# Kernel tuning notes

Measured on AMD Instinct MI355X. Metric: run time of the kernel, lower is better.

Reference implementation:

```python
import jax, jax.numpy as jnp
import numpy as np

N, T, D, H = 128, 128, 1024, 1024


def setup_inputs() -> dict:
    key = jax.random.key(0)
    ks = jax.random.split(key, 5)
    x = jax.random.normal(ks[0], (N, T, D), dtype=jnp.float32)
    A = jax.random.normal(ks[1], (N, H, 4, 4), dtype=jnp.float32)
    Wx = jax.random.normal(ks[2], (D, 4 * H), dtype=jnp.float32) / np.sqrt(D)
    Wh = jax.random.normal(ks[3], (H, 4 * H), dtype=jnp.float32) / np.sqrt(H)
    Wattn = jax.random.normal(ks[4], (H, 4 * H), dtype=jnp.float32) / np.sqrt(H)
    b = jnp.zeros((4 * H,), dtype=jnp.float32)
    return {"x": x, "A": A, "Wx": Wx, "Wh": Wh, "Wattn": Wattn, "b": b}


def reference(x, A, Wx, Wh, Wattn, b):
    n, t, d = x.shape
    h_dim = A.shape[1]
    scale = 1.0 / (h_dim ** 0.5)
    A_flat = A.reshape(n, h_dim, 16)            # (N, H, 16) flattened 4x4 grid
    h0 = A_flat.mean(axis=2)                    # mean-pooled feature init
    c0 = h0

    def step(carry, xt):
        h, c = carry
        # scaled dot-product attention over the 16 spatial positions
        scores = jnp.einsum('nh,nhp->np', h, A_flat) * scale   # (N, 16)
        w = jax.nn.softmax(scores, axis=-1)
        attn = jnp.einsum('nhp,np->nh', A_flat, w)             # (N, H)
        # fused gate pre-activations
        a = h @ Wh + xt @ Wx + attn @ Wattn + b                # (N, 4H)
        ai, af, ao, ag = jnp.split(a, 4, axis=1)
        i = jax.nn.sigmoid(ai)
        f = jax.nn.sigmoid(af)
        o = jax.nn.sigmoid(ao)
        g = jnp.tanh(ag)
        nc = f * c + i * g
        nh = o * jnp.tanh(nc)
        return (nh, nc), nh

    _, hs = jax.lax.scan(step, (h0, c0), jnp.transpose(x, (1, 0, 2)))
    return jnp.transpose(hs, (1, 0, 2))         # (N, T, H)
```

## Files before the change

kernel.cpp:

```cpp
#include <hip/hip_runtime.h>
#include <hip/hip_bf16.h>


typedef __bf16 bf16x8 __attribute__((ext_vector_type(8)));
typedef float f32x4 __attribute__((ext_vector_type(4)));

__device__ __forceinline__ unsigned short f2bf(float f) {
    unsigned int u = __float_as_uint(f);
    u += 0x7FFFu + ((u >> 16) & 1u);
    return (unsigned short)(u >> 16);
}
__device__ __forceinline__ float bf2f(unsigned short u) {
    return __uint_as_float(((unsigned int)u) << 16);
}
__device__ __forceinline__ float sigf(float x) { return 1.0f / (1.0f + __expf(-x)); }
__device__ __forceinline__ float tanhf_fast(float x) {
    const float t = __expf(-2.0f * fabsf(x));
    const float r = (1.0f - t) / (1.0f + t);
    return copysignf(r, x);
}

__global__ __launch_bounds__(256) void k_build_wtf2(
    const float* __restrict__ Wh, const float* __restrict__ Wx,
    unsigned short* __restrict__ WTf) {
    __shared__ float tile[64][65];
    const int cs2 = blockIdx.x;
    const int kq  = blockIdx.y;
    const int tid = threadIdx.x;
#pragma unroll
    for (int it = 0; it < 16; ++it) {
        int idx = it * 256 + tid;
        int kl = idx >> 6, cl = idx & 63;
        int col = cs2 * 64 + cl;
        int j = (col & 3) * 1024 + (col >> 2);
        int k = kq * 64 + kl;
        tile[kl][cl] = (k < 1024) ? Wh[(size_t)k * 4096 + j]
                                  : Wx[(size_t)(k - 1024) * 4096 + j];
    }
    __syncthreads();
#pragma unroll
    for (int it = 0; it < 2; ++it) {
        int slotid = it * 256 + tid;
        int l   = slotid & 63;
        int cf  = (slotid >> 6) & 1;
        int ksl = (slotid >> 7) & 1;
        int sl  = slotid >> 8;
        int s = cs2 * 2 + sl, ks = kq * 2 + ksl;
        int clocal = sl * 32 + cf * 16 + (l & 15);
        int klocal = ksl * 32 + ((l >> 4) << 3);
        unsigned short v[8];
#pragma unroll
        for (int i = 0; i < 8; ++i) v[i] = f2bf(tile[klocal + i][clocal]);
        *(int4*)&WTf[(size_t)(((s * 64 + ks) * 2 + cf) * 64 + l) * 8] = *(const int4*)v;
    }
}

__global__ __launch_bounds__(256) void k_build_waf(
    const float* __restrict__ Wattn, unsigned short* __restrict__ WAf) {
    __shared__ float tile[64][65];
    const int cs2 = blockIdx.x;
    const int kq  = blockIdx.y;
    const int tid = threadIdx.x;
#pragma unroll
    for (int it = 0; it < 16; ++it) {
        int idx = it * 256 + tid;
        int kl = idx >> 6, cl = idx & 63;
        int col = cs2 * 64 + cl;
        int j = (col & 3) * 1024 + (col >> 2);
        int k = kq * 64 + kl;
        tile[kl][cl] = Wattn[(size_t)k * 4096 + j];
    }
    __syncthreads();
#pragma unroll
    for (int it = 0; it < 2; ++it) {
        int slotid = it * 256 + tid;
        int l   = slotid & 63;
        int cf  = (slotid >> 6) & 1;
        int ksl = (slotid >> 7) & 1;
        int sl  = slotid >> 8;
        int s = cs2 * 2 + sl, ks = kq * 2 + ksl;
        int clocal = sl * 32 + cf * 16 + (l & 15);
        int klocal = ksl * 32 + ((l >> 4) << 3);
        unsigned short v[8];
#pragma unroll
        for (int i = 0; i < 8; ++i) v[i] = f2bf(tile[klocal + i][clocal]);
        *(int4*)&WAf[(size_t)(((s * 32 + ks) * 2 + cf) * 64 + l) * 8] = *(const int4*)v;
    }
}

__global__ __launch_bounds__(256) void k_pack_at(
    const float* __restrict__ Ag, unsigned short* __restrict__ ATf) {
    __shared__ unsigned short lds[1024][17];
    const int n = blockIdx.x;
    const int tid = threadIdx.x;
#pragma unroll
    for (int it = 0; it < 16; ++it) {
        int idx = it * 256 + tid;
        const float4 v = ((const float4*)(Ag + (size_t)n * 16384))[idx];
        int flat = idx * 4;
        int u = flat >> 4, p = flat & 15;
        lds[u][p + 0] = f2bf(v.x); lds[u][p + 1] = f2bf(v.y);
        lds[u][p + 2] = f2bf(v.z); lds[u][p + 3] = f2bf(v.w);
    }
    __syncthreads();
#pragma unroll
    for (int it = 0; it < 8; ++it) {
        int slot = it * 256 + tid;
        int kc = slot >> 6, l = slot & 63;
        int ubase = kc * 32 + ((l >> 4) << 3);
        int p = l & 15;
        unsigned short v[8];
#pragma unroll
        for (int i = 0; i < 8; ++i) v[i] = lds[ubase + i][p];
        *(int4*)&ATf[((size_t)n * 2048 + slot) * 8] = *(const int4*)v;
    }
}

__global__ __launch_bounds__(512) void k_aw_gemm(
    const unsigned short* __restrict__ ATf, const unsigned short* __restrict__ WAf,
    unsigned short* __restrict__ AW) {
    const int ng = blockIdx.x;
    const int ct = blockIdx.y;
    const int tid = threadIdx.x;
    const int lane = tid & 63, wave = tid >> 6;
    const int s = ct * 4 + (wave >> 1), cf = wave & 1;
    const int n0 = ng * 8;
    f32x4 acc[8] = {};
    const unsigned short* bp = WAf + ((size_t)((s * 32) * 2 + cf) * 64 + lane) * 8;
    const unsigned short* ap = ATf + ((size_t)n0 * 2048 + lane) * 8;
#pragma unroll 4
    for (int kc = 0; kc < 32; ++kc) {
        bf16x8 bf = *(const bf16x8*)(bp + (size_t)kc * 1024);
#pragma unroll
        for (int nn = 0; nn < 8; ++nn) {
            bf16x8 af = *(const bf16x8*)(ap + (size_t)nn * 16384 + (size_t)kc * 512);
            acc[nn] = __builtin_amdgcn_mfma_f32_16x16x32_bf16(af, bf, acc[nn], 0, 0, 0);
        }
    }
    const int col = ct * 128 + wave * 16 + (lane & 15);
    const int prow = (lane >> 4) << 2;
#pragma unroll
    for (int nn = 0; nn < 8; ++nn) {
        ushort4 st = make_ushort4(f2bf(acc[nn][0]), f2bf(acc[nn][1]),
                                  f2bf(acc[nn][2]), f2bf(acc[nn][3]));
        *(ushort4*)&AW[((size_t)(n0 + nn) * 4096 + col) * 16 + prow] = st;
    }
}

__global__ __launch_bounds__(512) void k_build_aw(
    const float* __restrict__ Wattn, const float* __restrict__ Ag,
    unsigned short* __restrict__ AW) {
    extern __shared__ float Alds[];
    const int jt = blockIdx.x;
    const int ng = blockIdx.y;
    const int tid = threadIdx.x;
    const int jl = tid & 127, pg = tid >> 7;
    const int jj = jt * 128 + jl;
    for (int nn = 0; nn < 16; ++nn) {
        const int n = ng * 16 + nn;
        __syncthreads();
#pragma unroll
        for (int q = 0; q < 8; ++q) {
            int idx = q * 512 + tid;
            ((float4*)Alds)[idx] = ((const float4*)(Ag + (size_t)n * 16384))[idx];
        }
        __syncthreads();
        f32x4 acc = {0.f, 0.f, 0.f, 0.f};
#pragma unroll 8
        for (int u = 0; u < 1024; ++u) {
            float wv = Wattn[(size_t)u * 4096 + jj];
            const float4 av = *(const float4*)&Alds[u * 16 + pg * 4];
            acc[0] += wv * av.x; acc[1] += wv * av.y;
            acc[2] += wv * av.z; acc[3] += wv * av.w;
        }
        const int g = jj >> 10, unit = jj & 1023;
        const int cre = unit * 4 + g;
        ushort4 st = make_ushort4(f2bf(acc[0]), f2bf(acc[1]), f2bf(acc[2]), f2bf(acc[3]));
        *(ushort4*)&AW[((size_t)n * 4096 + cre) * 16 + pg * 4] = st;
    }
}

__global__ __launch_bounds__(512) void k_init(
    const float* __restrict__ Ag, float* __restrict__ cst,
    unsigned short* __restrict__ hF0, float* __restrict__ sp) {
    const int n = blockIdx.x;
    const int t = threadIdx.x;
    float contrib[16];
#pragma unroll
    for (int p = 0; p < 16; ++p) contrib[p] = 0.f;
#pragma unroll
    for (int e = 0; e < 2; ++e) {
        const int u = t * 2 + e;
        const float4* ap = (const float4*)&Ag[((size_t)n * 1024 + u) * 16];
        float4 a0 = ap[0], a1 = ap[1], a2 = ap[2], a3 = ap[3];
        float s = a0.x + a0.y + a0.z + a0.w + a1.x + a1.y + a1.z + a1.w +
                  a2.x + a2.y + a2.z + a2.w + a3.x + a3.y + a3.z + a3.w;
        float h0 = s * (1.0f / 16.0f);
        cst[n * 1024 + u] = h0;
        const int rfg = n >> 4, kc = u >> 5, l = (n & 15) | (((u >> 3) & 3) << 4);
        hF0[(size_t)((rfg * 32 + kc) * 64 + l) * 8 + (u & 7)] = f2bf(h0);
        contrib[0]  += h0 * a0.x;  contrib[1]  += h0 * a0.y;
        contrib[2]  += h0 * a0.z;  contrib[3]  += h0 * a0.w;
        contrib[4]  += h0 * a1.x;  contrib[5]  += h0 * a1.y;
        contrib[6]  += h0 * a1.z;  contrib[7]  += h0 * a1.w;
        contrib[8]  += h0 * a2.x;  contrib[9]  += h0 * a2.y;
        contrib[10] += h0 * a2.z;  contrib[11] += h0 * a2.w;
        contrib[12] += h0 * a3.x;  contrib[13] += h0 * a3.y;
        contrib[14] += h0 * a3.z;  contrib[15] += h0 * a3.w;
    }
#pragma unroll
    for (int p = 0; p < 16; ++p) {
        contrib[p] += __shfl_xor(contrib[p], 1);
        contrib[p] += __shfl_xor(contrib[p], 2);
    }
    if ((t & 3) == 0) {
        const int slice = t >> 2;
        float4* dst = (float4*)&sp[(size_t)n * 4096 + slice * 16];
        dst[0] = make_float4(contrib[0], contrib[1], contrib[2], contrib[3]);
        dst[1] = make_float4(contrib[4], contrib[5], contrib[6], contrib[7]);
        dst[2] = make_float4(contrib[8], contrib[9], contrib[10], contrib[11]);
        dst[3] = make_float4(contrib[12], contrib[13], contrib[14], contrib[15]);
    }
    *(float4*)&sp[(size_t)n * 4096 + 2048 + t * 4] = make_float4(0.f, 0.f, 0.f, 0.f);
}

__global__ __launch_bounds__(64) void k_soft(
    const float* __restrict__ spin, float* __restrict__ w_ws,
    const float* __restrict__ x, unsigned short* __restrict__ xf, int ts) {
    __shared__ float sq[16];
    const int n = blockIdx.x;
    const int lane = threadIdx.x;
    f32x4 acc = {0.f, 0.f, 0.f, 0.f};
    const float4* base = (const float4*)(spin + (size_t)n * 4096);
#pragma unroll
    for (int it = 0; it < 16; ++it) {
        const float4 v = base[it * 64 + lane];
        acc[0] += v.x; acc[1] += v.y; acc[2] += v.z; acc[3] += v.w;
    }
#pragma unroll
    for (int m = 4; m <= 32; m <<= 1) {
        acc[0] += __shfl_xor(acc[0], m);
        acc[1] += __shfl_xor(acc[1], m);
        acc[2] += __shfl_xor(acc[2], m);
        acc[3] += __shfl_xor(acc[3], m);
    }
    if (lane < 4) *(float4*)&sq[lane * 4] = make_float4(acc[0], acc[1], acc[2], acc[3]);
    __syncthreads();
    if (lane < 16) {
        const float s = sq[lane] * 0.03125f;
        float mx = s;
#pragma unroll
        for (int m = 1; m < 16; m <<= 1) mx = fmaxf(mx, __shfl_xor(mx, m));
        const float e = __expf(s - mx);
        float se = e;
#pragma unroll
        for (int m = 1; m < 16; m <<= 1) se += __shfl_xor(se, m);
        w_ws[n * 16 + lane] = e / se;
    }
    const float4* xp = (const float4*)&x[((size_t)n * 128 + ts) * 1024];
#pragma unroll
    for (int i = 0; i < 2; ++i) {
        const int js = lane * 2 + i;
        const float4 x0 = xp[js * 2], x1 = xp[js * 2 + 1];
        unsigned short v[8] = {f2bf(x0.x), f2bf(x0.y), f2bf(x0.z), f2bf(x0.w),
                               f2bf(x1.x), f2bf(x1.y), f2bf(x1.z), f2bf(x1.w)};
        const int j0 = js * 8;
        const int l = (n & 15) | (((j0 >> 3) & 3) << 4);
        *(int4*)&xf[(size_t)(((n >> 4) * 32 + (j0 >> 5)) * 64 + l) * 8] = *(const int4*)v;
    }
}

__global__ __launch_bounds__(512, 4) void k_step(
    const unsigned short* __restrict__ WTf, const unsigned short* __restrict__ AW,
    const unsigned short* __restrict__ hFin, unsigned short* __restrict__ hFout,
    const unsigned short* __restrict__ xf,
    const float* __restrict__ w_ws, float* __restrict__ spout,
    float* __restrict__ cst, const float* __restrict__ Ag,
    const float* __restrict__ bias4, float* __restrict__ out, int ts) {
    __shared__ float wlds[64][17];
    __shared__ float accred[2048];
    const int bid0 = blockIdx.x;
    const int lid = (bid0 & 7) * 64 + (bid0 >> 3);
    const int cs16 = lid >> 1, rh = lid & 1;
    const int tid = threadIdx.x;
    const int lane = tid & 63, wave = tid >> 6;
    const int rf = wave >> 1, kh = wave & 1;

    f32x4 acc = {0.f, 0.f, 0.f, 0.f};
    {
        const unsigned short* ap = (kh == 0 ? hFin : xf)
            + ((size_t)((rh * 4 + rf) * 32) * 64 + lane) * 8;
        const unsigned short* bp = WTf
            + ((size_t)((((cs16 >> 1) * 64 + kh * 32) * 2) + (cs16 & 1)) * 64 + lane) * 8;
        bf16x8 ar[8], br[8];
#pragma unroll
        for (int i = 0; i < 8; ++i) {
            ar[i] = *(const bf16x8*)(ap + (size_t)i * 512);
            br[i] = *(const bf16x8*)(bp + (size_t)i * 1024);
        }
#pragma unroll
        for (int kb = 0; kb < 32; ++kb) {
            bf16x8 a = ar[kb & 7], b = br[kb & 7];
            if (kb < 24) {
                ar[kb & 7] = *(const bf16x8*)(ap + (size_t)(kb + 8) * 512);
                br[kb & 7] = *(const bf16x8*)(bp + (size_t)(kb + 8) * 1024);
            }
            acc = __builtin_amdgcn_mfma_f32_16x16x32_bf16(a, b, acc, 0, 0, 0);
        }
    }

    const int lq = lane & 15;
    const int hi = lane >> 4;
    const int mycol = cs16 * 16 + lq;
    const int u = mycol >> 2, g = mycol & 3;
    int4 aw0[2], aw1[2];
    float cold[2];
#pragma unroll
    for (int e = 0; e < 2; ++e) {
        const int reg = kh * 2 + e;
        const int r = rh * 64 + rf * 16 + hi * 4 + reg;
        const int4* awv = (const int4*)&AW[((size_t)r * 4096 + mycol) * 16];
        aw0[e] = awv[0];
        aw1[e] = awv[1];
        cold[e] = cst[r * 1024 + u];
    }
#pragma unroll
    for (int it = 0; it < 2; ++it) {
        const int idx = it * 512 + tid;
        wlds[idx >> 4][idx & 15] = w_ws[(rh * 64 + (idx >> 4)) * 16 + (idx & 15)];
    }
    *(f32x4*)&accred[(wave * 64 + lane) * 4] = acc;
    __syncthreads();
    acc += *(const f32x4*)&accred[(((rf << 1) | (kh ^ 1)) * 64 + lane) * 4];

    const float bias = bias4[g * 1024 + u];
    float nhv[2];
#pragma unroll
    for (int e = 0; e < 2; ++e) {
        const int reg = kh * 2 + e;
        const int r = rh * 64 + rf * 16 + hi * 4 + reg;
        const int rl = rf * 16 + hi * 4 + reg;
        union { int4 v; unsigned short us[8]; } a0u, a1u;
        a0u.v = aw0[e]; a1u.v = aw1[e];
        float aextra = 0.f;
#pragma unroll
        for (int p = 0; p < 8; ++p) aextra += wlds[rl][p] * bf2f(a0u.us[p]);
#pragma unroll
        for (int p = 0; p < 8; ++p) aextra += wlds[rl][8 + p] * bf2f(a1u.us[p]);
        float a = acc[reg] + bias + aextra;
        float v1 = __shfl_xor(a, 1);
        float v2 = __shfl_xor(a, 2);
        float v3 = __shfl_xor(a, 3);
        auto pick = [&](int m) { return m == 0 ? a : m == 1 ? v1 : m == 2 ? v2 : v3; };
        float ii = sigf(pick(g));
        float ff = sigf(pick(g ^ 1));
        float oo = sigf(pick(g ^ 2));
        float gg = tanhf_fast(pick(g ^ 3));
        const float nc = ff * cold[e] + ii * gg;
        const float nh = oo * tanhf_fast(nc);
        nhv[e] = nh;
        if (g == 0) {
            cst[r * 1024 + u] = nc;
        } else if (g == 1) {
            hFout[(size_t)(((r >> 4) * 32 + (u >> 5)) * 64 +
                           ((r & 15) | (((u >> 3) & 3) << 4))) * 8 + (u & 7)] = f2bf(nh);
        } else if (g == 3) {
            out[((size_t)r * 128 + ts) * 1024 + u] = nh;
        }
    }
    if ((lq & 3) == 2) {
#pragma unroll
        for (int e = 0; e < 2; ++e) {
            const int reg = kh * 2 + e;
            const int r = rh * 64 + rf * 16 + hi * 4 + reg;
            const float nh = nhv[e];
            const float4* Ap = (const float4*)&Ag[((size_t)r * 1024 + u) * 16];
            float contrib[16];
#pragma unroll
            for (int q = 0; q < 4; ++q) {
                const float4 cv = Ap[q];
                contrib[q * 4 + 0] = nh * cv.x;
                contrib[q * 4 + 1] = nh * cv.y;
                contrib[q * 4 + 2] = nh * cv.z;
                contrib[q * 4 + 3] = nh * cv.w;
            }
#pragma unroll
            for (int p = 0; p < 16; ++p) {
                contrib[p] += __shfl_xor(contrib[p], 4);
                contrib[p] += __shfl_xor(contrib[p], 8);
            }
            if (lq == 2) {
                float4* dst = (float4*)&spout[((size_t)r * 256 + cs16) * 16];
                dst[0] = make_float4(contrib[0], contrib[1], contrib[2], contrib[3]);
                dst[1] = make_float4(contrib[4], contrib[5], contrib[6], contrib[7]);
                dst[2] = make_float4(contrib[8], contrib[9], contrib[10], contrib[11]);
                dst[3] = make_float4(contrib[12], contrib[13], contrib[14], contrib[15]);
            }
        }
    }
}

extern "C" void kernel_launch(void* const* d_in, const int* in_sizes, int n_in,
                              void* d_out, int out_size, void* d_ws, size_t ws_size,
                              hipStream_t stream) {
    const float* x     = (const float*)d_in[0];
    const float* A     = (const float*)d_in[1];
    const float* Wx    = (const float*)d_in[2];
    const float* Wh    = (const float*)d_in[3];
    const float* Wattn = (const float*)d_in[4];
    const float* b     = (const float*)d_in[5];
    float* out = (float*)d_out;

    char* ws = (char*)d_ws;
    unsigned short* WTf = (unsigned short*)(ws);
    unsigned short* AW  = (unsigned short*)(ws + 16777216);
    unsigned short* hF0 = (unsigned short*)(ws + 33554432);
    unsigned short* hF1 = (unsigned short*)(ws + 33816576);
    unsigned short* xf  = (unsigned short*)(ws + 34078720);
    float* cst  = (float*)(ws + 34340864);
    float* w_ws = (float*)(ws + 34865152);
    float* sp0  = (float*)(ws + 34873344);
    float* sp1  = (float*)(ws + 36970496);
    unsigned short* ATf = (unsigned short*)(ws + 33554432);
    unsigned short* WAf = (unsigned short*)(ws + 37748736);

    k_build_wtf2<<<dim3(64, 32), 256, 0, stream>>>(Wh, Wx, WTf);
    if (ws_size >= 46137344u) {
        k_build_waf<<<dim3(64, 16), 256, 0, stream>>>(Wattn, WAf);
        k_pack_at<<<128, 256, 0, stream>>>(A, ATf);
        k_aw_gemm<<<dim3(16, 32), 512, 0, stream>>>(ATf, WAf, AW);
    } else {
        k_build_aw<<<dim3(32, 8), 512, 65536, stream>>>(Wattn, A, AW);
    }
    k_init<<<128, 512, 0, stream>>>(A, cst, hF0, sp0);

    for (int ts = 0; ts < 128; ++ts) {
        unsigned short* hin  = (ts & 1) ? hF1 : hF0;
        unsigned short* hout = (ts & 1) ? hF0 : hF1;
        float* spin  = (ts & 1) ? sp1 : sp0;
        float* spout = (ts & 1) ? sp0 : sp1;
        k_soft<<<128, 64, 0, stream>>>(spin, w_ws, x, xf, ts);
        k_step<<<512, 512, 0, stream>>>(WTf, AW, hin, hout, xf,
                                        w_ws, spout, cst, A, b, out, ts);
    }
}
```

Measured before the change: 2.661 ms.

## Fold softmax and x conversion into step kernel using atomic score accumulation

Removes the per-timestep k_soft launch. Each step block now computes the 16-way softmax redundantly from a reduced score buffer, and reduces the next step's attention scores directly with atomicAdd into a triple-rotated buffer that is zeroed one step ahead. The bf16 packing of the next timestep's x is done at the tail of k_step into a double-buffered xf. This halves the launch count and removes the partial-score buffer, at the cost of float atomics, which make the sums non-deterministic, and of redundant softmax work in every block.

New measurement: 4.760 ms. +78.9%, slower.

```diff
diff --git a/kernel.cpp b/kernel.cpp
--- a/kernel.cpp
+++ b/kernel.cpp
@@ -181,10 +181,22 @@
 }
 
 __global__ __launch_bounds__(512) void k_init(
-    const float* __restrict__ Ag, float* __restrict__ cst,
-    unsigned short* __restrict__ hF0, float* __restrict__ sp) {
+    const float* __restrict__ Ag, const float* __restrict__ x,
+    float* __restrict__ cst, unsigned short* __restrict__ hF0,
+    unsigned short* __restrict__ xf0,
+    float* __restrict__ s0, float* __restrict__ s1, float* __restrict__ s2) {
+    __shared__ float wpart[8][16];
     const int n = blockIdx.x;
     const int t = threadIdx.x;
+    if (t < 128) {
+        const int j0 = t * 8;
+        const float4* xp = (const float4*)&x[((size_t)n * 128 + 0) * 1024 + j0];
+        float4 x0 = xp[0], x1 = xp[1];
+        unsigned short v[8] = {f2bf(x0.x), f2bf(x0.y), f2bf(x0.z), f2bf(x0.w),
+                               f2bf(x1.x), f2bf(x1.y), f2bf(x1.z), f2bf(x1.w)};
+        const int rfg = n >> 4, kc = j0 >> 5, l = (n & 15) | (((j0 >> 3) & 3) << 4);
+        *(int4*)&xf0[(size_t)((rfg * 32 + kc) * 64 + l) * 8] = *(const int4*)v;
+    }
     float contrib[16];
 #pragma unroll
     for (int p = 0; p < 16; ++p) contrib[p] = 0.f;
@@ -210,73 +222,33 @@
     }
 #pragma unroll
     for (int p = 0; p < 16; ++p) {
-        contrib[p] += __shfl_xor(contrib[p], 1);
-        contrib[p] += __shfl_xor(contrib[p], 2);
-    }
-    if ((t & 3) == 0) {
-        const int slice = t >> 2;
-        float4* dst = (float4*)&sp[(size_t)n * 4096 + slice * 16];
-        dst[0] = make_float4(contrib[0], contrib[1], contrib[2], contrib[3]);
-        dst[1] = make_float4(contrib[4], contrib[5], contrib[6], contrib[7]);
-        dst[2] = make_float4(contrib[8], contrib[9], contrib[10], contrib[11]);
-        dst[3] = make_float4(contrib[12], contrib[13], contrib[14], contrib[15]);
-    }
-    *(float4*)&sp[(size_t)n * 4096 + 2048 + t * 4] = make_float4(0.f, 0.f, 0.f, 0.f);
-}
-
-__global__ __launch_bounds__(64) void k_soft(
-    const float* __restrict__ spin, float* __restrict__ w_ws,
-    const float* __restrict__ x, unsigned short* __restrict__ xf, int ts) {
-    __shared__ float sq[16];
-    const int n = blockIdx.x;
-    const int lane = threadIdx.x;
-    f32x4 acc = {0.f, 0.f, 0.f, 0.f};
-    const float4* base = (const float4*)(spin + (size_t)n * 4096);
-#pragma unroll
-    for (int it = 0; it < 16; ++it) {
-        const float4 v = base[it * 64 + lane];
-        acc[0] += v.x; acc[1] += v.y; acc[2] += v.z; acc[3] += v.w;
-    }
-#pragma unroll
-    for (int m = 4; m <= 32; m <<= 1) {
-        acc[0] += __shfl_xor(acc[0], m);
-        acc[1] += __shfl_xor(acc[1], m);
-        acc[2] += __shfl_xor(acc[2], m);
-        acc[3] += __shfl_xor(acc[3], m);
-    }
-    if (lane < 4) *(float4*)&sq[lane * 4] = make_float4(acc[0], acc[1], acc[2], acc[3]);
+#pragma unroll
+        for (int m = 1; m <= 32; m <<= 1) contrib[p] += __shfl_xor(contrib[p], m);
+    }
+    if ((t & 63) == 0) {
+#pragma unroll
+        for (int p = 0; p < 16; ++p) wpart[t >> 6][p] = contrib[p];
+    }
     __syncthreads();
-    if (lane < 16) {
-        const float s = sq[lane] * 0.03125f;
-        float mx = s;
-#pragma unroll
-        for (int m = 1; m < 16; m <<= 1) mx = fmaxf(mx, __shfl_xor(mx, m));
-        const float e = __expf(s - mx);
-        float se = e;
-#pragma unroll
-        for (int m = 1; m < 16; m <<= 1) se += __shfl_xor(se, m);
-        w_ws[n * 16 + lane] = e / se;
-    }
-    const float4* xp = (const float4*)&x[((size_t)n * 128 + ts) * 1024];
-#pragma unroll
-    for (int i = 0; i < 2; ++i) {
-        const int js = lane * 2 + i;
-        const float4 x0 = xp[js * 2], x1 = xp[js * 2 + 1];
-        unsigned short v[8] = {f2bf(x0.x), f2bf(x0.y), f2bf(x0.z), f2bf(x0.w),
-                               f2bf(x1.x), f2bf(x1.y), f2bf(x1.z), f2bf(x1.w)};
-        const int j0 = js * 8;
-        const int l = (n & 15) | (((j0 >> 3) & 3) << 4);
-        *(int4*)&xf[(size_t)(((n >> 4) * 32 + (j0 >> 5)) * 64 + l) * 8] = *(const int4*)v;
+    if (t < 16) {
+        float s = 0.f;
+#pragma unroll
+        for (int w = 0; w < 8; ++w) s += wpart[w][t];
+        s0[n * 16 + t] = s;
+        s1[n * 16 + t] = 0.f;
+        s2[n * 16 + t] = 0.f;
     }
 }
 
 __global__ __launch_bounds__(512, 4) void k_step(
     const unsigned short* __restrict__ WTf, const unsigned short* __restrict__ AW,
     const unsigned short* __restrict__ hFin, unsigned short* __restrict__ hFout,
-    const unsigned short* __restrict__ xf,
-    const float* __restrict__ w_ws, float* __restrict__ spout,
+    const unsigned short* __restrict__ xfin, unsigned short* __restrict__ xfout,
+    const float* __restrict__ sread, float* __restrict__ saccum,
+    float* __restrict__ szero,
     float* __restrict__ cst, const float* __restrict__ Ag,
-    const float* __restrict__ bias4, float* __restrict__ out, int ts) {
+    const float* __restrict__ x, const float* __restrict__ bias4,
+    float* __restrict__ out, int ts) {
     __shared__ float wlds[64][17];
     __shared__ float accred[2048];
     const int bid0 = blockIdx.x;
@@ -286,9 +258,25 @@
     const int lane = tid & 63, wave = tid >> 6;
     const int rf = wave >> 1, kh = wave & 1;
 
+    if (tid == 0) *(float4*)&szero[bid0 * 4] = make_float4(0.f, 0.f, 0.f, 0.f);
+#pragma unroll
+    for (int it = 0; it < 2; ++it) {
+        const int idx = it * 512 + tid;
+        const int rl = idx >> 4, p = idx & 15;
+        const float sv = sread[(rh * 64 + rl) * 16 + p] * 0.03125f;
+        float mx = sv;
+#pragma unroll
+        for (int m = 1; m < 16; m <<= 1) mx = fmaxf(mx, __shfl_xor(mx, m));
+        const float e = __expf(sv - mx);
+        float se = e;
+#pragma unroll
+        for (int m = 1; m < 16; m <<= 1) se += __shfl_xor(se, m);
+        wlds[rl][p] = e / se;
+    }
+
     f32x4 acc = {0.f, 0.f, 0.f, 0.f};
     {
-        const unsigned short* ap = (kh == 0 ? hFin : xf)
+        const unsigned short* ap = (kh == 0 ? hFin : xfin)
             + ((size_t)((rh * 4 + rf) * 32) * 64 + lane) * 8;
         const unsigned short* bp = WTf
             + ((size_t)((((cs16 >> 1) * 64 + kh * 32) * 2) + (cs16 & 1)) * 64 + lane) * 8;
@@ -323,11 +311,6 @@
         aw0[e] = awv[0];
         aw1[e] = awv[1];
         cold[e] = cst[r * 1024 + u];
-    }
-#pragma unroll
-    for (int it = 0; it < 2; ++it) {
-        const int idx = it * 512 + tid;
-        wlds[idx >> 4][idx & 15] = w_ws[(rh * 64 + (idx >> 4)) * 16 + (idx & 15)];
     }
     *(f32x4*)&accred[(wave * 64 + lane) * 4] = acc;
     __syncthreads();
@@ -389,14 +372,21 @@
                 contrib[p] += __shfl_xor(contrib[p], 4);
                 contrib[p] += __shfl_xor(contrib[p], 8);
             }
-            if (lq == 2) {
-                float4* dst = (float4*)&spout[((size_t)r * 256 + cs16) * 16];
-                dst[0] = make_float4(contrib[0], contrib[1], contrib[2], contrib[3]);
-                dst[1] = make_float4(contrib[4], contrib[5], contrib[6], contrib[7]);
-                dst[2] = make_float4(contrib[8], contrib[9], contrib[10], contrib[11]);
-                dst[3] = make_float4(contrib[12], contrib[13], contrib[14], contrib[15]);
-            }
-        }
+            const int pbase = (lq >> 2) * 4;
+#pragma unroll
+            for (int pp = 0; pp < 4; ++pp)
+                atomicAdd(&saccum[r * 16 + pbase + pp], contrib[pbase + pp]);
+        }
+    }
+    if (ts + 1 < 128 && tid < 32) {
+        const int slot = bid0 * 32 + tid;
+        const int n = slot >> 7, js = slot & 127, j0 = js * 8;
+        const float4* xp = (const float4*)&x[((size_t)n * 128 + (ts + 1)) * 1024 + j0];
+        float4 x0 = xp[0], x1 = xp[1];
+        unsigned short v[8] = {f2bf(x0.x), f2bf(x0.y), f2bf(x0.z), f2bf(x0.w),
+                               f2bf(x1.x), f2bf(x1.y), f2bf(x1.z), f2bf(x1.w)};
+        const int rfg2 = n >> 4, kc = j0 >> 5, l = (n & 15) | (((j0 >> 3) & 3) << 4);
+        *(int4*)&xfout[(size_t)((rfg2 * 32 + kc) * 64 + l) * 8] = *(const int4*)v;
     }
 }
 
@@ -416,11 +406,10 @@
     unsigned short* AW  = (unsigned short*)(ws + 16777216);
     unsigned short* hF0 = (unsigned short*)(ws + 33554432);
     unsigned short* hF1 = (unsigned short*)(ws + 33816576);
-    unsigned short* xf  = (unsigned short*)(ws + 34078720);
-    float* cst  = (float*)(ws + 34340864);
-    float* w_ws = (float*)(ws + 34865152);
-    float* sp0  = (float*)(ws + 34873344);
-    float* sp1  = (float*)(ws + 36970496);
+    unsigned short* xfA = (unsigned short*)(ws + 34078720);
+    unsigned short* xfB = (unsigned short*)(ws + 34340864);
+    float* cst  = (float*)(ws + 34603008);
+    float* sbuf = (float*)(ws + 35127296);
     unsigned short* ATf = (unsigned short*)(ws + 33554432);
     unsigned short* WAf = (unsigned short*)(ws + 37748736);
 
@@ -432,15 +421,19 @@
     } else {
         k_build_aw<<<dim3(32, 8), 512, 65536, stream>>>(Wattn, A, AW);
     }
-    k_init<<<128, 512, 0, stream>>>(A, cst, hF0, sp0);
+    k_init<<<128, 512, 0, stream>>>(A, x, cst, hF0, xfA,
+                                    sbuf, sbuf + 2048, sbuf + 4096);
 
     for (int ts = 0; ts < 128; ++ts) {
         unsigned short* hin  = (ts & 1) ? hF1 : hF0;
         unsigned short* hout = (ts & 1) ? hF0 : hF1;
-        float* spin  = (ts & 1) ? sp1 : sp0;
-        float* spout = (ts & 1) ? sp0 : sp1;
-        k_soft<<<128, 64, 0, stream>>>(spin, w_ws, x, xf, ts);
-        k_step<<<512, 512, 0, stream>>>(WTf, AW, hin, hout, xf,
-                                        w_ws, spout, cst, A, b, out, ts);
-    }
-}
+        unsigned short* xin  = (ts & 1) ? xfB : xfA;
+        unsigned short* xout = (ts & 1) ? xfA : xfB;
+        float* sread  = sbuf + (size_t)(ts % 3) * 2048;
+        float* saccum = sbuf + (size_t)((ts + 1) % 3) * 2048;
+        float* szero  = sbuf + (size_t)((ts + 2) % 3) * 2048;
+        k_step<<<512, 512, 0, stream>>>(WTf, AW, hin, hout, xin, xout,
+                                        sread, saccum, szero,
+                                        cst, A, x, b, out, ts);
+    }
+}
```

## Hoist x@Wx into chunked batched GEMM and halve per-step recurrent GEMM work

Applied to the files above, without the earlier changes.

The input projection x@Wx is taken out of the sequential step kernel and computed every 8 timesteps by a separate MFMA GEMM that converts x to bf16 on the fly and stores xWc in bf16. The step kernel then only multiplies h by Wh (K=1024 instead of 2048), uses 256 blocks with 4 rows per lane, and drops the LDS cross-wave reduction. The spin/spout double buffer is merged into a single sp buffer and the fallback AW path is removed. This gives the per-step critical path less work in exchange for extra launches, bf16 rounding of xWx, and a possible read/write hazard on the shared sp buffer.

After: 4.124 ms. +55.0%, slower.

```diff
diff --git a/kernel.cpp b/kernel.cpp
--- a/kernel.cpp
+++ b/kernel.cpp
@@ -20,9 +20,8 @@
     return copysignf(r, x);
 }
 
-__global__ __launch_bounds__(256) void k_build_wtf2(
-    const float* __restrict__ Wh, const float* __restrict__ Wx,
-    unsigned short* __restrict__ WTf) {
+__global__ __launch_bounds__(256) void k_build_wf(
+    const float* __restrict__ W, unsigned short* __restrict__ WF) {
     __shared__ float tile[64][65];
     const int cs2 = blockIdx.x;
     const int kq  = blockIdx.y;
@@ -34,8 +33,7 @@
         int col = cs2 * 64 + cl;
         int j = (col & 3) * 1024 + (col >> 2);
         int k = kq * 64 + kl;
-        tile[kl][cl] = (k < 1024) ? Wh[(size_t)k * 4096 + j]
-                                  : Wx[(size_t)(k - 1024) * 4096 + j];
+        tile[kl][cl] = W[(size_t)k * 4096 + j];
     }
     __syncthreads();
 #pragma unroll
@@ -51,40 +49,7 @@
         unsigned short v[8];
 #pragma unroll
         for (int i = 0; i < 8; ++i) v[i] = f2bf(tile[klocal + i][clocal]);
-        *(int4*)&WTf[(size_t)(((s * 64 + ks) * 2 + cf) * 64 + l) * 8] = *(const int4*)v;
-    }
-}
-
-__global__ __launch_bounds__(256) void k_build_waf(
-    const float* __restrict__ Wattn, unsigned short* __restrict__ WAf) {
-    __shared__ float tile[64][65];
-    const int cs2 = blockIdx.x;
-    const int kq  = blockIdx.y;
-    const int tid = threadIdx.x;
-#pragma unroll
-    for (int it = 0; it < 16; ++it) {
-        int idx = it * 256 + tid;
-        int kl = idx >> 6, cl = idx & 63;
-        int col = cs2 * 64 + cl;
-        int j = (col & 3) * 1024 + (col >> 2);
-        int k = kq * 64 + kl;
-        tile[kl][cl] = Wattn[(size_t)k * 4096 + j];
-    }
-    __syncthreads();
-#pragma unroll
-    for (int it = 0; it < 2; ++it) {
-        int slotid = it * 256 + tid;
-        int l   = slotid & 63;
-        int cf  = (slotid >> 6) & 1;
-        int ksl = (slotid >> 7) & 1;
-        int sl  = slotid >> 8;
-        int s = cs2 * 2 + sl, ks = kq * 2 + ksl;
-        int clocal = sl * 32 + cf * 16 + (l & 15);
-        int klocal = ksl * 32 + ((l >> 4) << 3);
-        unsigned short v[8];
-#pragma unroll
-        for (int i = 0; i < 8; ++i) v[i] = f2bf(tile[klocal + i][clocal]);
-        *(int4*)&WAf[(size_t)(((s * 32 + ks) * 2 + cf) * 64 + l) * 8] = *(const int4*)v;
+        *(int4*)&WF[(size_t)(((s * 32 + ks) * 2 + cf) * 64 + l) * 8] = *(const int4*)v;
     }
 }
 
@@ -147,36 +112,42 @@
     }
 }
 
-__global__ __launch_bounds__(512) void k_build_aw(
-    const float* __restrict__ Wattn, const float* __restrict__ Ag,
-    unsigned short* __restrict__ AW) {
-    extern __shared__ float Alds[];
-    const int jt = blockIdx.x;
-    const int ng = blockIdx.y;
-    const int tid = threadIdx.x;
-    const int jl = tid & 127, pg = tid >> 7;
-    const int jj = jt * 128 + jl;
-    for (int nn = 0; nn < 16; ++nn) {
-        const int n = ng * 16 + nn;
-        __syncthreads();
-#pragma unroll
-        for (int q = 0; q < 8; ++q) {
-            int idx = q * 512 + tid;
-            ((float4*)Alds)[idx] = ((const float4*)(Ag + (size_t)n * 16384))[idx];
-        }
-        __syncthreads();
-        f32x4 acc = {0.f, 0.f, 0.f, 0.f};
-#pragma unroll 8
-        for (int u = 0; u < 1024; ++u) {
-            float wv = Wattn[(size_t)u * 4096 + jj];
-            const float4 av = *(const float4*)&Alds[u * 16 + pg * 4];
-            acc[0] += wv * av.x; acc[1] += wv * av.y;
-            acc[2] += wv * av.z; acc[3] += wv * av.w;
-        }
-        const int g = jj >> 10, unit = jj & 1023;
-        const int cre = unit * 4 + g;
-        ushort4 st = make_ushort4(f2bf(acc[0]), f2bf(acc[1]), f2bf(acc[2]), f2bf(acc[3]));
-        *(ushort4*)&AW[((size_t)n * 4096 + cre) * 16 + pg * 4] = st;
+__global__ __launch_bounds__(512, 2) void k_xw_gemm(
+    const float* __restrict__ x, const unsigned short* __restrict__ WxF,
+    unsigned short* __restrict__ xWc, int t0) {
+    const int rt = blockIdx.x;
+    const int ct = blockIdx.y;
+    const int tid = threadIdx.x;
+    const int lane = tid & 63, wave = tid >> 6;
+    const int s = ct * 4 + (wave >> 1), cf = wave & 1;
+    const int lq = lane & 15, hi = lane >> 4;
+    const int tg = t0 + rt;
+    const float* xb[8];
+#pragma unroll
+    for (int rfg = 0; rfg < 8; ++rfg)
+        xb[rfg] = x + ((size_t)(rfg * 16 + lq) * 128 + tg) * 1024 + hi * 8;
+    const unsigned short* bp = WxF + ((size_t)((s * 32) * 2 + cf) * 64 + lane) * 8;
+    f32x4 acc[8] = {};
+#pragma unroll 2
+    for (int kc = 0; kc < 32; ++kc) {
+        bf16x8 bfr = *(const bf16x8*)(bp + (size_t)kc * 1024);
+#pragma unroll
+        for (int rfg = 0; rfg < 8; ++rfg) {
+            const float4* xp = (const float4*)(xb[rfg] + kc * 32);
+            const float4 v0 = xp[0], v1 = xp[1];
+            unsigned short us[8] = {f2bf(v0.x), f2bf(v0.y), f2bf(v0.z), f2bf(v0.w),
+                                    f2bf(v1.x), f2bf(v1.y), f2bf(v1.z), f2bf(v1.w)};
+            bf16x8 af = *(const bf16x8*)us;
+            acc[rfg] = __builtin_amdgcn_mfma_f32_16x16x32_bf16(af, bfr, acc[rfg], 0, 0, 0);
+        }
+    }
+    const int col = ct * 128 + wave * 16 + lq;
+#pragma unroll
+    for (int rfg = 0; rfg < 8; ++rfg) {
+        const int nn0 = rfg * 16 + hi * 4;
+        ushort4 st = make_ushort4(f2bf(acc[rfg][0]), f2bf(acc[rfg][1]),
+                                  f2bf(acc[rfg][2]), f2bf(acc[rfg][3]));
+        *(ushort4*)&xWc[((size_t)rt * 4096 + col) * 128 + nn0] = st;
     }
 }
 
@@ -225,8 +196,7 @@
 }
 
 __global__ __launch_bounds__(64) void k_soft(
-    const float* __restrict__ spin, float* __restrict__ w_ws,
-    const float* __restrict__ x, unsigned short* __restrict__ xf, int ts) {
+    const float* __restrict__ spin, float* __restrict__ w_ws) {
     __shared__ float sq[16];
     const int n = blockIdx.x;
     const int lane = threadIdx.x;
@@ -257,41 +227,33 @@
         for (int m = 1; m < 16; m <<= 1) se += __shfl_xor(se, m);
         w_ws[n * 16 + lane] = e / se;
     }
-    const float4* xp = (const float4*)&x[((size_t)n * 128 + ts) * 1024];
-#pragma unroll
-    for (int i = 0; i < 2; ++i) {
-        const int js = lane * 2 + i;
-        const float4 x0 = xp[js * 2], x1 = xp[js * 2 + 1];
-        unsigned short v[8] = {f2bf(x0.x), f2bf(x0.y), f2bf(x0.z), f2bf(x0.w),
-                               f2bf(x1.x), f2bf(x1.y), f2bf(x1.z), f2bf(x1.w)};
-        const int j0 = js * 8;
-        const int l = (n & 15) | (((j0 >> 3) & 3) << 4);
-        *(int4*)&xf[(size_t)(((n >> 4) * 32 + (j0 >> 5)) * 64 + l) * 8] = *(const int4*)v;
-    }
-}
-
-__global__ __launch_bounds__(512, 4) void k_step(
-    const unsigned short* __restrict__ WTf, const unsigned short* __restrict__ AW,
+}
+
+__global__ __launch_bounds__(512, 2) void k_step(
+    const unsigned short* __restrict__ WhF, const unsigned short* __restrict__ AW,
     const unsigned short* __restrict__ hFin, unsigned short* __restrict__ hFout,
-    const unsigned short* __restrict__ xf,
+    const unsigned short* __restrict__ xWc,
     const float* __restrict__ w_ws, float* __restrict__ spout,
     float* __restrict__ cst, const float* __restrict__ Ag,
     const float* __restrict__ bias4, float* __restrict__ out, int ts) {
-    __shared__ float wlds[64][17];
-    __shared__ float accred[2048];
+    __shared__ float wlds[128][17];
     const int bid0 = blockIdx.x;
-    const int lid = (bid0 & 7) * 64 + (bid0 >> 3);
-    const int cs16 = lid >> 1, rh = lid & 1;
+    const int cs16 = (bid0 & 7) * 32 + (bid0 >> 3);
     const int tid = threadIdx.x;
     const int lane = tid & 63, wave = tid >> 6;
-    const int rf = wave >> 1, kh = wave & 1;
+
+#pragma unroll
+    for (int it = 0; it < 4; ++it) {
+        const int idx = it * 512 + tid;
+        wlds[idx >> 4][idx & 15] = w_ws[idx];
+    }
+    __syncthreads();
 
     f32x4 acc = {0.f, 0.f, 0.f, 0.f};
     {
-        const unsigned short* ap = (kh == 0 ? hFin : xf)
-            + ((size_t)((rh * 4 + rf) * 32) * 64 + lane) * 8;
-        const unsigned short* bp = WTf
-            + ((size_t)((((cs16 >> 1) * 64 + kh * 32) * 2) + (cs16 & 1)) * 64 + lane) * 8;
+        const unsigned short* ap = hFin + ((size_t)(wave * 32) * 64 + lane) * 8;
+        const unsigned short* bp = WhF
+            + ((size_t)(((cs16 >> 1) * 32) * 2 + (cs16 & 1)) * 64 + lane) * 8;
         bf16x8 ar[8], br[8];
 #pragma unroll
         for (int i = 0; i < 8; ++i) {
@@ -309,45 +271,36 @@
         }
     }
 
-    const int lq = lane & 15;
-    const int hi = lane >> 4;
+    const int lq = lane & 15, hi = lane >> 4;
     const int mycol = cs16 * 16 + lq;
     const int u = mycol >> 2, g = mycol & 3;
-    int4 aw0[2], aw1[2];
-    float cold[2];
-#pragma unroll
-    for (int e = 0; e < 2; ++e) {
-        const int reg = kh * 2 + e;
-        const int r = rh * 64 + rf * 16 + hi * 4 + reg;
+    const int r0 = wave * 16 + hi * 4;
+    int4 aw0[4], aw1[4];
+    float cold[4];
+#pragma unroll
+    for (int e = 0; e < 4; ++e) {
+        const int r = r0 + e;
         const int4* awv = (const int4*)&AW[((size_t)r * 4096 + mycol) * 16];
         aw0[e] = awv[0];
         aw1[e] = awv[1];
         cold[e] = cst[r * 1024 + u];
     }
-#pragma unroll
-    for (int it = 0; it < 2; ++it) {
-        const int idx = it * 512 + tid;
-        wlds[idx >> 4][idx & 15] = w_ws[(rh * 64 + (idx >> 4)) * 16 + (idx & 15)];
-    }
-    *(f32x4*)&accred[(wave * 64 + lane) * 4] = acc;
-    __syncthreads();
-    acc += *(const f32x4*)&accred[(((rf << 1) | (kh ^ 1)) * 64 + lane) * 4];
-
+    const ushort4 xwv = *(const ushort4*)&xWc[((size_t)(ts & 7) * 4096 + mycol) * 128 + r0];
+    const unsigned short* xwe = (const unsigned short*)&xwv;
     const float bias = bias4[g * 1024 + u];
-    float nhv[2];
-#pragma unroll
-    for (int e = 0; e < 2; ++e) {
-        const int reg = kh * 2 + e;
-        const int r = rh * 64 + rf * 16 + hi * 4 + reg;
-        const int rl = rf * 16 + hi * 4 + reg;
+
+    float nhv[4];
+#pragma unroll
+    for (int e = 0; e < 4; ++e) {
+        const int r = r0 + e;
         union { int4 v; unsigned short us[8]; } a0u, a1u;
         a0u.v = aw0[e]; a1u.v = aw1[e];
         float aextra = 0.f;
 #pragma unroll
-        for (int p = 0; p < 8; ++p) aextra += wlds[rl][p] * bf2f(a0u.us[p]);
-#pragma unroll
-        for (int p = 0; p < 8; ++p) aextra += wlds[rl][8 + p] * bf2f(a1u.us[p]);
-        float a = acc[reg] + bias + aextra;
+        for (int p = 0; p < 8; ++p) aextra += wlds[r][p] * bf2f(a0u.us[p]);
+#pragma unroll
+        for (int p = 0; p < 8; ++p) aextra += wlds[r][8 + p] * bf2f(a1u.us[p]);
+        float a = acc[e] + bias + aextra + bf2f(xwe[e]);
         float v1 = __shfl_xor(a, 1);
         float v2 = __shfl_xor(a, 2);
         float v3 = __shfl_xor(a, 3);
@@ -370,9 +323,8 @@
     }
     if ((lq & 3) == 2) {
 #pragma unroll
-        for (int e = 0; e < 2; ++e) {
-            const int reg = kh * 2 + e;
-            const int r = rh * 64 + rf * 16 + hi * 4 + reg;
+        for (int e = 0; e < 4; ++e) {
+            const int r = r0 + e;
             const float nh = nhv[e];
             const float4* Ap = (const float4*)&Ag[((size_t)r * 1024 + u) * 16];
             float contrib[16];
@@ -412,35 +364,32 @@
     float* out = (float*)d_out;
 
     char* ws = (char*)d_ws;
-    unsigned short* WTf = (unsigned short*)(ws);
-    unsigned short* AW  = (unsigned short*)(ws + 16777216);
-    unsigned short* hF0 = (unsigned short*)(ws + 33554432);
-    unsigned short* hF1 = (unsigned short*)(ws + 33816576);
-    unsigned short* xf  = (unsigned short*)(ws + 34078720);
-    float* cst  = (float*)(ws + 34340864);
-    float* w_ws = (float*)(ws + 34865152);
-    float* sp0  = (float*)(ws + 34873344);
-    float* sp1  = (float*)(ws + 36970496);
-    unsigned short* ATf = (unsigned short*)(ws + 33554432);
-    unsigned short* WAf = (unsigned short*)(ws + 37748736);
-
-    k_build_wtf2<<<dim3(64, 32), 256, 0, stream>>>(Wh, Wx, WTf);
-    if (ws_size >= 46137344u) {
-        k_build_waf<<<dim3(64, 16), 256, 0, stream>>>(Wattn, WAf);
-        k_pack_at<<<128, 256, 0, stream>>>(A, ATf);
-        k_aw_gemm<<<dim3(16, 32), 512, 0, stream>>>(ATf, WAf, AW);
-    } else {
-        k_build_aw<<<dim3(32, 8), 512, 65536, stream>>>(Wattn, A, AW);
-    }
-    k_init<<<128, 512, 0, stream>>>(A, cst, hF0, sp0);
+    unsigned short* WhF = (unsigned short*)(ws);
+    unsigned short* AW  = (unsigned short*)(ws + 8388608);
+    unsigned short* WxF = (unsigned short*)(ws + 25165824);
+    unsigned short* xWc = (unsigned short*)(ws + 33554432);
+    unsigned short* hF0 = (unsigned short*)(ws + 41943040);
+    unsigned short* hF1 = (unsigned short*)(ws + 42205184);
+    float* cst  = (float*)(ws + 42467328);
+    float* w_ws = (float*)(ws + 42991616);
+    float* sp   = (float*)(ws + 42999808);
+    unsigned short* WAf = (unsigned short*)(ws + 33554432);
+    unsigned short* ATf = (unsigned short*)(ws + 41943040);
+
+    k_build_wf<<<dim3(64, 16), 256, 0, stream>>>(Wh, WhF);
+    k_build_wf<<<dim3(64, 16), 256, 0, stream>>>(Wattn, WAf);
+    k_build_wf<<<dim3(64, 16), 256, 0, stream>>>(Wx, WxF);
+    k_pack_at<<<128, 256, 0, stream>>>(A, ATf);
+    k_aw_gemm<<<dim3(16, 32), 512, 0, stream>>>(ATf, WAf, AW);
+    k_init<<<128, 512, 0, stream>>>(A, cst, hF0, sp);
 
     for (int ts = 0; ts < 128; ++ts) {
+        if ((ts & 7) == 0)
+            k_xw_gemm<<<dim3(8, 32), 512, 0, stream>>>(x, WxF, xWc, ts);
         unsigned short* hin  = (ts & 1) ? hF1 : hF0;
         unsigned short* hout = (ts & 1) ? hF0 : hF1;
-        float* spin  = (ts & 1) ? sp1 : sp0;
-        float* spout = (ts & 1) ? sp0 : sp1;
-        k_soft<<<128, 64, 0, stream>>>(spin, w_ws, x, xf, ts);
-        k_step<<<512, 512, 0, stream>>>(WTf, AW, hin, hout, xf,
-                                        w_ws, spout, cst, A, b, out, ts);
-    }
-}
+        k_soft<<<128, 64, 0, stream>>>(sp, w_ws);
+        k_step<<<256, 512, 0, stream>>>(WhF, AW, hin, hout, xWc,
+                                        w_ws, sp, cst, A, b, out, ts);
+    }
+}
```
